# Performance work log

Hardware: AMD Instinct MI355X
Metric: run time of the kernel (lower is better)

The kernel has to match this reference:

```python
import jax, jax.numpy as jnp
import numpy as np
from math import factorial

ZS = np.array([0, 1])
NZ = 2
N_BASIS = 3
N_CHAN = N_BASIS * N_BASIS
N_RBF = 8
MAX_L = 3
CUTOFF = 5.5
P_CUT = 6
N_NODES = 10000
N_EDGES = 100000


def _lxlylz_list(max_l):
    out = []
    for l in range(max_l + 1):
        for lx in range(l, -1, -1):
            for ly in range(l - lx, -1, -1):
                out.append((lx, ly, l - lx - ly))
    return out

LXLYLZ = np.array(_lxlylz_list(MAX_L), dtype=np.int32)  # [n_ang, 3]; (0,0,0) is index 0
N_ANG = LXLYLZ.shape[0]  # 20 for max_l=3

# nu=2 rotational invariants: for each l>0, monomial indices with lx+ly+lz==l and multinomial prefactors
NU2 = []
for l in range(1, MAX_L + 1):
    idx = [i for i in range(N_ANG) if int(LXLYLZ[i].sum()) == l]
    pref = np.array([factorial(l) / (factorial(int(LXLYLZ[i][0])) * factorial(int(LXLYLZ[i][1])) * factorial(int(LXLYLZ[i][2]))) for i in idx], dtype=np.float32)
    NU2.append((np.array(idx, dtype=np.int32), pref))


def setup_inputs() -> dict:
    key = jax.random.key(0)
    ks = jax.random.split(key, 6)
    positions = jax.random.normal(ks[0], (N_NODES, 3), jnp.float32)
    atomic_numbers = jax.random.randint(ks[1], (N_NODES,), 0, NZ)
    edge_index = jax.random.randint(ks[2], (2, N_EDGES), 0, N_NODES)
    edge_lengths = jax.random.uniform(ks[3], (N_EDGES,), jnp.float32, 0.5, CUTOFF)
    edge_vectors = jax.random.normal(ks[4], (N_EDGES, 3), jnp.float32)
    W_embed = jax.random.normal(ks[5], (NZ, N_BASIS), jnp.float32) / np.sqrt(NZ)
    return dict(positions=positions, atomic_numbers=atomic_numbers, edge_index=edge_index,
                edge_lengths=edge_lengths, edge_vectors=edge_vectors, W_embed=W_embed)


def reference(positions, atomic_numbers, edge_index, edge_lengths, edge_vectors, W_embed):
    n_nodes = positions.shape[0]
    # node one-hot over zs -> linear embedding
    one_hot = (atomic_numbers[:, None] == jnp.asarray(ZS)[None, :]).astype(W_embed.dtype)
    emb = one_hot @ W_embed  # [N, n_basis]
    # directed edge-type encoding: outer product of sender/receiver embeddings
    enc = (emb[edge_index[0]][:, :, None] * emb[edge_index[1]][:, None, :]).reshape(-1, N_CHAN)  # [E, c]
    # Bessel radial basis * polynomial cutoff
    r = edge_lengths
    n = jnp.arange(1, N_RBF + 1, dtype=r.dtype)
    radial = jnp.sqrt(2.0 / CUTOFF) * jnp.sin(n[None, :] * jnp.pi * r[:, None] / CUTOFF) / r[:, None]
    u = r / CUTOFF
    p = P_CUT
    fc = (1.0 - 0.5 * (p + 1) * (p + 2) * u ** p + p * (p + 2) * u ** (p + 1)
          - 0.5 * p * (p + 1) * u ** (p + 2)) * (u < 1.0)
    radial = radial * fc[:, None]  # [E, n_rbf]
    # angular monomials x^lx y^ly z^lz of unit edge vectors
    unit = edge_vectors / jnp.linalg.norm(edge_vectors, axis=-1, keepdims=True)
    ang = jnp.prod(unit[:, None, :] ** jnp.asarray(LXLYLZ)[None, :, :], axis=-1)  # [E, n_ang]
    # fused 3-tensor edge product then scatter-sum to receiver nodes
    edge_attr = jnp.einsum('er,ea,ec->erac', radial, ang, enc)  # [E, n_rbf, n_ang, c]
    A = jax.ops.segment_sum(edge_attr, edge_index[1], num_segments=n_nodes)  # node_feat_A
    # symmetrize to invariants: nu=1 (l=0 monomial) + nu=2 per-l invariants
    feats = [A[:, :, 0:1, :]]
    for idx, pref in NU2:
        sel = A[:, :, jnp.asarray(idx), :]
        feats.append(jnp.sum(jnp.asarray(pref)[None, None, :, None] * sel * sel, axis=2, keepdims=True))
    B = jnp.concatenate(feats, axis=2)  # node_feat_B: [N, n_rbf, 1+max_l, c]
    return B
```

## Files before the change

kernel.cpp:

```cpp
#include <hip/hip_runtime.h>


#define NN    10000
#define NE    100000
#define NRBF  8
#define NANG  20
#define NCHAN 9
#define CAP   64
#define BROW  28
#define NODES_PER_BLK 4
#define INV_CUT  (1.0f/5.5f)
#define PI_F     3.14159265358979323846f
#define RAD_NORM 0.6030226891555273f

#define WSYNC() asm volatile("s_waitcnt lgkmcnt(0)" ::: "memory")

__launch_bounds__(256, 4)
__global__ void scatter_k(const int* __restrict__ an, const int* __restrict__ ei,
                          int* __restrict__ cnt, int* __restrict__ lst) {
    int e = blockIdx.x * blockDim.x + threadIdx.x;
    if (e >= NE) return;
    int src = ei[e];
    int dst = ei[NE + e];
    int zs  = an[src];
    int pos = atomicAdd(&cnt[dst], 1);
    if (pos < CAP) lst[dst * CAP + pos] = e | (zs << 20);
}

__launch_bounds__(256, 5)
__global__ void node_k(const int* __restrict__ an, const float* __restrict__ elen,
                       const float* __restrict__ evec, const float* __restrict__ W,
                       const int* __restrict__ cnt, const int* __restrict__ lst,
                       float* __restrict__ out)
{
    __shared__ float sB[NODES_PER_BLK * CAP * BROW];

    const int tid  = threadIdx.x;
    const int w    = tid >> 6;
    const int lane = tid & 63;
    const int n    = blockIdx.x * NODES_PER_BLK + w;

    float* Bw = &sB[w * CAP * BROW];

    const int vv  = lst[n * CAP + lane];
    const int dgr = cnt[n];
    const int zd  = an[n];
    const float Wa0=W[0], Wa1=W[1], Wa2=W[2], Wa3=W[3], Wa4=W[4], Wa5=W[5];

    const int deg = (dgr > CAP) ? CAP : dgr;

    int zsv = 0;
    if (lane < deg) {
        const int eid = vv & 0xFFFFF;
        zsv = vv >> 20;

        const float r  = elen[eid];
        const float vx = evec[3*eid+0], vy = evec[3*eid+1], vz = evec[3*eid+2];
        const float inv = rsqrtf(vx*vx + vy*vy + vz*vz);
        const float x = vx*inv, y = vy*inv, z = vz*inv;

        const float u  = r * INV_CUT;
        const float u2 = u*u, u6 = u2*u2*u2;
        const float fc = (u < 1.0f) ? (1.0f - 28.0f*u6 + 48.0f*u6*u - 21.0f*u6*u2)
                                    : 0.0f;
        const float scale = RAD_NORM * fc / r;
        float s1, c1;
        sincosf(PI_F * u, &s1, &c1);
        const float twoc = 2.0f * c1;
        float sp = 0.0f, s = s1;
        float rad[8];
        #pragma unroll
        for (int k = 0; k < 8; ++k) {
            rad[k] = scale * s;
            const float sn = twoc * s - sp;
            sp = s; s = sn;
        }

        const float xx = x*x, xy = x*y, xz = x*z, yy = y*y, yz = y*z, zz = z*z;
        float* B = &Bw[lane * BROW];
        *(float4*)&B[0]  = make_float4(rad[0], rad[1], rad[2], rad[3]);
        *(float4*)&B[4]  = make_float4(rad[4], rad[5], rad[6], rad[7]);
        *(float4*)&B[8]  = make_float4(1.0f, x, y, z);
        *(float4*)&B[12] = make_float4(xx, xy, xz, yy);
        *(float4*)&B[16] = make_float4(yz, zz, x*xx, y*xx);
        *(float4*)&B[20] = make_float4(z*xx, x*yy, x*yz, x*zz);
        *(float4*)&B[24] = make_float4(y*yy, z*yy, y*zz, z*zz);
    }
    const unsigned long long zmask = __ballot(zsv != 0);
    WSYNC();

    const int r0 = lane & 7;
    const int a0 = lane >> 3;
    float s00=0.f, s01=0.f, s02=0.f;
    float s10=0.f, s11=0.f, s12=0.f;

    int e = 0;
    for (; e + 1 < deg; e += 2) {
        const float* Ba = &Bw[e * BROW];
        const float* Bb = &Bw[(e+1) * BROW];
        const float z1a = (float)((zmask >> e) & 1ULL);
        const float z1b = (float)((zmask >> (e+1)) & 1ULL);
        const float z0a = 1.0f - z1a, z0b = 1.0f - z1b;
        const float rda = Ba[r0],      rdb = Bb[r0];
        const float v0a = rda * Ba[8 + a0],  v0b = rdb * Bb[8 + a0];
        const float v1a = rda * Ba[16 + a0], v1b = rdb * Bb[16 + a0];
        s00 = fmaf(v0a, z0a, s00); s10 = fmaf(v0a, z1a, s10);
        s01 = fmaf(v1a, z0a, s01); s11 = fmaf(v1a, z1a, s11);
        s00 = fmaf(v0b, z0b, s00); s10 = fmaf(v0b, z1b, s10);
        s01 = fmaf(v1b, z0b, s01); s11 = fmaf(v1b, z1b, s11);
        if (lane < 32) {
            const float v2a = rda * Ba[24 + a0], v2b = rdb * Bb[24 + a0];
            s02 = fmaf(v2a, z0a, s02); s12 = fmaf(v2a, z1a, s12);
            s02 = fmaf(v2b, z0b, s02); s12 = fmaf(v2b, z1b, s12);
        }
    }
    if (e < deg) {
        const float* B = &Bw[e * BROW];
        const float z1 = (float)((zmask >> e) & 1ULL);
        const float z0 = 1.0f - z1;
        const float rd = B[r0];
        const float v0 = rd * B[8 + a0];
        const float v1 = rd * B[16 + a0];
        s00 = fmaf(v0, z0, s00); s10 = fmaf(v0, z1, s10);
        s01 = fmaf(v1, z0, s01); s11 = fmaf(v1, z1, s11);
        if (lane < 32) {
            const float v2 = rd * B[24 + a0];
            s02 = fmaf(v2, z0, s02); s12 = fmaf(v2, z1, s12);
        }
    }

    const float pf0 = (float)((0x12211110u >> (4*a0)) & 0xF);
    const float pf1 = (float)((0x36333112u >> (4*a0)) & 0xF);
    const float pf2 = (float)((0x1331u     >> (4*a0)) & 0xF);

    const float WL[3] = {Wa0, Wa1, Wa2};
    const float WH[3] = {Wa3, Wa4, Wa5};
    float T0k[3], b1[3], b2[3], b3[3];
    #pragma unroll
    for (int i = 0; i < 3; ++i) {
        const float T0 = WL[i]*s00 + WH[i]*s10;
        const float T1 = WL[i]*s01 + WH[i]*s11;
        const float T2 = WL[i]*s02 + WH[i]*s12;
        T0k[i] = T0;
        const float q0 = pf0 * T0 * T0;
        const float q1 = pf1 * T1 * T1;
        const float q2 = pf2 * T2 * T2;
        b1[i] = (a0 >= 1 && a0 <= 3) ? q0 : 0.f;
        b2[i] = ((a0 >= 4) ? q0 : 0.f) + ((a0 <= 1) ? q1 : 0.f);
        b3[i] = ((a0 >= 2) ? q1 : 0.f) + q2;
    }

    #pragma unroll
    for (int m = 8; m <= 32; m <<= 1) {
        #pragma unroll
        for (int i = 0; i < 3; ++i) {
            b1[i] += __shfl_xor(b1[i], m, 64);
            b2[i] += __shfl_xor(b2[i], m, 64);
            b3[i] += __shfl_xor(b3[i], m, 64);
        }
    }

    if (lane < 8) {
        const float wd0 = zd ? Wa3 : Wa0, wd1 = zd ? Wa4 : Wa1, wd2 = zd ? Wa5 : Wa2;
        const float e0 = wd0*wd0, e1 = wd1*wd1, e2 = wd2*wd2;
        float v[36];
        #pragma unroll
        for (int i = 0; i < 3; ++i) {
            v[     i*3+0] = T0k[i]*wd0; v[     i*3+1] = T0k[i]*wd1; v[     i*3+2] = T0k[i]*wd2;
            v[ 9 + i*3+0] = b1[i]*e0;   v[ 9 + i*3+1] = b1[i]*e1;   v[ 9 + i*3+2] = b1[i]*e2;
            v[18 + i*3+0] = b2[i]*e0;   v[18 + i*3+1] = b2[i]*e1;   v[18 + i*3+2] = b2[i]*e2;
            v[27 + i*3+0] = b3[i]*e0;   v[27 + i*3+1] = b3[i]*e1;   v[27 + i*3+2] = b3[i]*e2;
        }
        float4* O = (float4*)(out + (long)n * (NRBF*4*NCHAN) + lane * 36);
        #pragma unroll
        for (int k = 0; k < 9; ++k)
            O[k] = make_float4(v[4*k], v[4*k+1], v[4*k+2], v[4*k+3]);
    }
}

extern "C" void kernel_launch(void* const* d_in, const int* in_sizes, int n_in,
                              void* d_out, int out_size, void* d_ws, size_t ws_size,
                              hipStream_t stream) {
    const int*   an   = (const int*)d_in[1];
    const int*   ei   = (const int*)d_in[2];
    const float* elen = (const float*)d_in[3];
    const float* evec = (const float*)d_in[4];
    const float* W    = (const float*)d_in[5];
    float* out = (float*)d_out;

    int* cnt = (int*)d_ws;
    int* lst = cnt + NN;

    hipMemsetAsync(cnt, 0, NN * sizeof(int), stream);
    scatter_k<<<(NE + 255)/256, 256, 0, stream>>>(an, ei, cnt, lst);
    node_k<<<NN / NODES_PER_BLK, 256, 0, stream>>>(an, elen, evec, W, cnt, lst, out);
}
```

Baseline: 87.84 us.

## Process two nodes per wavefront with half-wave edge chunks

Each 64-lane wavefront now handles two nodes, one per 32-lane half. Edges are staged into shared memory in chunks of 32 per node and looped over up to the larger of the two degrees. Each lane accumulates five angular slices instead of three, and the shuffle reduction shrinks to within the half-wave. This targets idle lanes, since average degree is about 10 so most of a 64-lane edge slot went unused. In exchange it adds per-lane accumulation work, a chunk loop, and zero-fill writes for empty slots.

```diff
diff --git a/kernel.cpp b/kernel.cpp
--- a/kernel.cpp
+++ b/kernel.cpp
@@ -7,8 +7,9 @@
 #define NANG  20
 #define NCHAN 9
 #define CAP   64
+#define HCAP  32
 #define BROW  28
-#define NODES_PER_BLK 4
+#define NODES_PER_BLK 8
 #define INV_CUT  (1.0f/5.5f)
 #define PI_F     3.14159265358979323846f
 #define RAD_NORM 0.6030226891555273f
@@ -27,131 +28,126 @@
     if (pos < CAP) lst[dst * CAP + pos] = e | (zs << 20);
 }
 
-__launch_bounds__(256, 5)
+__launch_bounds__(256, 4)
 __global__ void node_k(const int* __restrict__ an, const float* __restrict__ elen,
                        const float* __restrict__ evec, const float* __restrict__ W,
                        const int* __restrict__ cnt, const int* __restrict__ lst,
                        float* __restrict__ out)
 {
-    __shared__ float sB[NODES_PER_BLK * CAP * BROW];
+    __shared__ float sB[4 * 64 * BROW];
 
     const int tid  = threadIdx.x;
     const int w    = tid >> 6;
     const int lane = tid & 63;
-    const int n    = blockIdx.x * NODES_PER_BLK + w;
+    const int half = lane >> 5;
+    const int hl   = lane & 31;
+    const int node = blockIdx.x * NODES_PER_BLK + 2*w + half;
 
-    float* Bw = &sB[w * CAP * BROW];
+    float* Bw = &sB[w * 64 * BROW];
 
-    const int vv  = lst[n * CAP + lane];
-    const int dgr = cnt[n];
-    const int zd  = an[n];
+    const int vv0 = lst[node * CAP + hl];
+    const int dgr = cnt[node];
+    const int zd  = an[node];
     const float Wa0=W[0], Wa1=W[1], Wa2=W[2], Wa3=W[3], Wa4=W[4], Wa5=W[5];
 
     const int deg = (dgr > CAP) ? CAP : dgr;
+    const int degA = __shfl(deg, 0, 64), degB = __shfl(deg, 32, 64);
+    const int maxdeg = (degA > degB) ? degA : degB;
 
-    int zsv = 0;
-    if (lane < deg) {
-        const int eid = vv & 0xFFFFF;
-        zsv = vv >> 20;
+    const int r0 = hl & 7;
+    const int a0 = hl >> 3;
+    float s0[5] = {0,0,0,0,0};
+    float s1[5] = {0,0,0,0,0};
 
-        const float r  = elen[eid];
-        const float vx = evec[3*eid+0], vy = evec[3*eid+1], vz = evec[3*eid+2];
-        const float inv = rsqrtf(vx*vx + vy*vy + vz*vz);
-        const float x = vx*inv, y = vy*inv, z = vz*inv;
+    for (int base = 0; base < maxdeg; base += HCAP) {
+        if (base) WSYNC();
+        const int vv = base ? lst[node * CAP + base + hl] : vv0;
+        float* B = &Bw[(half*HCAP + hl) * BROW];
+        int zsv = 0;
+        if (base + hl < deg) {
+            const int eid = vv & 0xFFFFF;
+            zsv = vv >> 20;
 
-        const float u  = r * INV_CUT;
-        const float u2 = u*u, u6 = u2*u2*u2;
-        const float fc = (u < 1.0f) ? (1.0f - 28.0f*u6 + 48.0f*u6*u - 21.0f*u6*u2)
-                                    : 0.0f;
-        const float scale = RAD_NORM * fc / r;
-        float s1, c1;
-        sincosf(PI_F * u, &s1, &c1);
-        const float twoc = 2.0f * c1;
-        float sp = 0.0f, s = s1;
-        float rad[8];
-        #pragma unroll
-        for (int k = 0; k < 8; ++k) {
-            rad[k] = scale * s;
-            const float sn = twoc * s - sp;
-            sp = s; s = sn;
+            const float r  = elen[eid];
+            const float vx = evec[3*eid+0], vy = evec[3*eid+1], vz = evec[3*eid+2];
+            const float inv = rsqrtf(vx*vx + vy*vy + vz*vz);
+            const float x = vx*inv, y = vy*inv, z = vz*inv;
+
+            const float u  = r * INV_CUT;
+            const float u2 = u*u, u6 = u2*u2*u2;
+            const float fc = (u < 1.0f)
+                           ? (1.0f - 28.0f*u6 + 48.0f*u6*u - 21.0f*u6*u2) : 0.0f;
+            const float scale = RAD_NORM * fc / r;
+            float sv, cv;
+            sincosf(PI_F * u, &sv, &cv);
+            const float twoc = 2.0f * cv;
+            float sp = 0.0f, s = sv;
+            float rad[8];
+            #pragma unroll
+            for (int k = 0; k < 8; ++k) {
+                rad[k] = scale * s;
+                const float sn = twoc * s - sp;
+                sp = s; s = sn;
+            }
+
+            const float xx = x*x, xy = x*y, xz = x*z, yy = y*y, yz = y*z, zz = z*z;
+            *(float4*)&B[0]  = make_float4(rad[0], rad[1], rad[2], rad[3]);
+            *(float4*)&B[4]  = make_float4(rad[4], rad[5], rad[6], rad[7]);
+            *(float4*)&B[8]  = make_float4(1.0f, x, y, z);
+            *(float4*)&B[12] = make_float4(xx, xy, xz, yy);
+            *(float4*)&B[16] = make_float4(yz, zz, x*xx, y*xx);
+            *(float4*)&B[20] = make_float4(z*xx, x*yy, x*yz, x*zz);
+            *(float4*)&B[24] = make_float4(y*yy, z*yy, y*zz, z*zz);
+        } else {
+            const float4 z4 = make_float4(0.f, 0.f, 0.f, 0.f);
+            *(float4*)&B[0]  = z4; *(float4*)&B[4]  = z4;
+            *(float4*)&B[8]  = z4; *(float4*)&B[12] = z4;
+            *(float4*)&B[16] = z4; *(float4*)&B[20] = z4;
+            *(float4*)&B[24] = z4;
         }
+        const unsigned long long zm = __ballot(zsv != 0);
+        WSYNC();
 
-        const float xx = x*x, xy = x*y, xz = x*z, yy = y*y, yz = y*z, zz = z*z;
-        float* B = &Bw[lane * BROW];
-        *(float4*)&B[0]  = make_float4(rad[0], rad[1], rad[2], rad[3]);
-        *(float4*)&B[4]  = make_float4(rad[4], rad[5], rad[6], rad[7]);
-        *(float4*)&B[8]  = make_float4(1.0f, x, y, z);
-        *(float4*)&B[12] = make_float4(xx, xy, xz, yy);
-        *(float4*)&B[16] = make_float4(yz, zz, x*xx, y*xx);
-        *(float4*)&B[20] = make_float4(z*xx, x*yy, x*yz, x*zz);
-        *(float4*)&B[24] = make_float4(y*yy, z*yy, y*zz, z*zz);
-    }
-    const unsigned long long zmask = __ballot(zsv != 0);
-    WSYNC();
-
-    const int r0 = lane & 7;
-    const int a0 = lane >> 3;
-    float s00=0.f, s01=0.f, s02=0.f;
-    float s10=0.f, s11=0.f, s12=0.f;
-
-    int e = 0;
-    for (; e + 1 < deg; e += 2) {
-        const float* Ba = &Bw[e * BROW];
-        const float* Bb = &Bw[(e+1) * BROW];
-        const float z1a = (float)((zmask >> e) & 1ULL);
-        const float z1b = (float)((zmask >> (e+1)) & 1ULL);
-        const float z0a = 1.0f - z1a, z0b = 1.0f - z1b;
-        const float rda = Ba[r0],      rdb = Bb[r0];
-        const float v0a = rda * Ba[8 + a0],  v0b = rdb * Bb[8 + a0];
-        const float v1a = rda * Ba[16 + a0], v1b = rdb * Bb[16 + a0];
-        s00 = fmaf(v0a, z0a, s00); s10 = fmaf(v0a, z1a, s10);
-        s01 = fmaf(v1a, z0a, s01); s11 = fmaf(v1a, z1a, s11);
-        s00 = fmaf(v0b, z0b, s00); s10 = fmaf(v0b, z1b, s10);
-        s01 = fmaf(v1b, z0b, s01); s11 = fmaf(v1b, z1b, s11);
-        if (lane < 32) {
-            const float v2a = rda * Ba[24 + a0], v2b = rdb * Bb[24 + a0];
-            s02 = fmaf(v2a, z0a, s02); s12 = fmaf(v2a, z1a, s12);
-            s02 = fmaf(v2b, z0b, s02); s12 = fmaf(v2b, z1b, s12);
-        }
-    }
-    if (e < deg) {
-        const float* B = &Bw[e * BROW];
-        const float z1 = (float)((zmask >> e) & 1ULL);
-        const float z0 = 1.0f - z1;
-        const float rd = B[r0];
-        const float v0 = rd * B[8 + a0];
-        const float v1 = rd * B[16 + a0];
-        s00 = fmaf(v0, z0, s00); s10 = fmaf(v0, z1, s10);
-        s01 = fmaf(v1, z0, s01); s11 = fmaf(v1, z1, s11);
-        if (lane < 32) {
-            const float v2 = rd * B[24 + a0];
-            s02 = fmaf(v2, z0, s02); s12 = fmaf(v2, z1, s12);
+        const int bound = (maxdeg - base < HCAP) ? (maxdeg - base) : HCAP;
+        const float* Bh = &Bw[half * HCAP * BROW];
+        for (int e = 0; e < bound; ++e) {
+            const float* Br = &Bh[e * BROW];
+            const float z1 = (float)((zm >> (half*32 + e)) & 1ULL);
+            const float z0 = 1.0f - z1;
+            const float rd = Br[r0];
+            float v;
+            v = rd * Br[ 8 + a0]; s0[0]=fmaf(v,z0,s0[0]); s1[0]=fmaf(v,z1,s1[0]);
+            v = rd * Br[12 + a0]; s0[1]=fmaf(v,z0,s0[1]); s1[1]=fmaf(v,z1,s1[1]);
+            v = rd * Br[16 + a0]; s0[2]=fmaf(v,z0,s0[2]); s1[2]=fmaf(v,z1,s1[2]);
+            v = rd * Br[20 + a0]; s0[3]=fmaf(v,z0,s0[3]); s1[3]=fmaf(v,z1,s1[3]);
+            v = rd * Br[24 + a0]; s0[4]=fmaf(v,z0,s0[4]); s1[4]=fmaf(v,z1,s1[4]);
         }
     }
 
-    const float pf0 = (float)((0x12211110u >> (4*a0)) & 0xF);
-    const float pf1 = (float)((0x36333112u >> (4*a0)) & 0xF);
-    const float pf2 = (float)((0x1331u     >> (4*a0)) & 0xF);
+    const float pf1 = (float)((0x1221u >> (4*a0)) & 0xF);
+    const float pf2 = (float)((0x3112u >> (4*a0)) & 0xF);
+    const float pf3 = (float)((0x3633u >> (4*a0)) & 0xF);
+    const float pf4 = (float)((0x1331u >> (4*a0)) & 0xF);
 
     const float WL[3] = {Wa0, Wa1, Wa2};
     const float WH[3] = {Wa3, Wa4, Wa5};
     float T0k[3], b1[3], b2[3], b3[3];
     #pragma unroll
     for (int i = 0; i < 3; ++i) {
-        const float T0 = WL[i]*s00 + WH[i]*s10;
-        const float T1 = WL[i]*s01 + WH[i]*s11;
-        const float T2 = WL[i]*s02 + WH[i]*s12;
+        const float T0 = WL[i]*s0[0] + WH[i]*s1[0];
+        const float T1 = WL[i]*s0[1] + WH[i]*s1[1];
+        const float T2 = WL[i]*s0[2] + WH[i]*s1[2];
+        const float T3 = WL[i]*s0[3] + WH[i]*s1[3];
+        const float T4 = WL[i]*s0[4] + WH[i]*s1[4];
         T0k[i] = T0;
-        const float q0 = pf0 * T0 * T0;
-        const float q1 = pf1 * T1 * T1;
         const float q2 = pf2 * T2 * T2;
-        b1[i] = (a0 >= 1 && a0 <= 3) ? q0 : 0.f;
-        b2[i] = ((a0 >= 4) ? q0 : 0.f) + ((a0 <= 1) ? q1 : 0.f);
-        b3[i] = ((a0 >= 2) ? q1 : 0.f) + q2;
+        b1[i] = (a0 >= 1) ? T0*T0 : 0.f;
+        b2[i] = pf1*T1*T1 + ((a0 <= 1) ? q2 : 0.f);
+        b3[i] = ((a0 >= 2) ? q2 : 0.f) + pf3*T3*T3 + pf4*T4*T4;
     }
 
     #pragma unroll
-    for (int m = 8; m <= 32; m <<= 1) {
+    for (int m = 8; m <= 16; m <<= 1) {
         #pragma unroll
         for (int i = 0; i < 3; ++i) {
             b1[i] += __shfl_xor(b1[i], m, 64);
@@ -160,7 +156,7 @@
         }
     }
 
-    if (lane < 8) {
+    if (hl < 8) {
         const float wd0 = zd ? Wa3 : Wa0, wd1 = zd ? Wa4 : Wa1, wd2 = zd ? Wa5 : Wa2;
         const float e0 = wd0*wd0, e1 = wd1*wd1, e2 = wd2*wd2;
         float v[36];
@@ -171,7 +167,7 @@
             v[18 + i*3+0] = b2[i]*e0;   v[18 + i*3+1] = b2[i]*e1;   v[18 + i*3+2] = b2[i]*e2;
             v[27 + i*3+0] = b3[i]*e0;   v[27 + i*3+1] = b3[i]*e1;   v[27 + i*3+2] = b3[i]*e2;
         }
-        float4* O = (float4*)(out + (long)n * (NRBF*4*NCHAN) + lane * 36);
+        float4* O = (float4*)(out + (long)node * (NRBF*4*NCHAN) + r0 * 36);
         #pragma unroll
         for (int k = 0; k < 9; ++k)
             O[k] = make_float4(v[4*k], v[4*k+1], v[4*k+2], v[4*k+3]);
```

New measurement: 84.77 us. 1.04x faster.
